# Kernel optimization log

Hardware: AMD Instinct MI355X
Metric: run time of the kernel (lower is better)

## Reference

```python
import jax, jax.numpy as jnp
import numpy as np

HEADS = 20


def _sdpa(q, k, v):
    # q: [B,H,Sq,D], k/v: [B,H,Sk,D]
    scale = 1.0 / jnp.sqrt(jnp.asarray(q.shape[-1], q.dtype))
    scores = jnp.einsum('bhqd,bhkd->bhqk', q, k) * scale
    probs = jax.nn.softmax(scores, axis=-1)
    return jnp.einsum('bhqk,bhkd->bhqd', probs, v)


def _split_heads(x, B, H):
    # [B,S,H*D] -> [B,H,S,D]
    S = x.shape[1]
    D = x.shape[2] // H
    return x.reshape(B, S, H, D).transpose(0, 2, 1, 3)


def setup_inputs() -> dict:
    key = jax.random.key(0)
    ks = jax.random.split(key, 10)
    B, S, C = 4, 4096, 1280
    T, Lid, X = 77, 32, 2048
    sc = lambda fan_in: 1.0 / np.sqrt(fan_in)
    return {
        'hidden_states': jax.random.normal(ks[0], (B, S, C), jnp.float32),
        'encoder_hidden_states': jax.random.normal(ks[1], (B, T, X), jnp.float32),
        'id_embedding': jax.random.normal(ks[2], (B, Lid, X), jnp.float32),
        'Wq': jax.random.normal(ks[3], (C, C), jnp.float32) * sc(C),
        'Wk': jax.random.normal(ks[4], (C, X), jnp.float32) * sc(X),
        'Wv': jax.random.normal(ks[5], (C, X), jnp.float32) * sc(X),
        'Wik': jax.random.normal(ks[6], (C, X), jnp.float32) * sc(X),
        'Wiv': jax.random.normal(ks[7], (C, X), jnp.float32) * sc(X),
        'Wo': jax.random.normal(ks[8], (C, C), jnp.float32) * sc(C),
        'bo': jnp.zeros((C,), jnp.float32),
    }


def reference(hidden_states, encoder_hidden_states, id_embedding,
              Wq, Wk, Wv, Wik, Wiv, Wo, bo):
    id_scale = 1.0
    B, S, C = hidden_states.shape
    H = HEADS
    residual = hidden_states

    q = _split_heads(hidden_states @ Wq.T, B, H)              # [B,H,S,D]
    k = _split_heads(encoder_hidden_states @ Wk.T, B, H)      # [B,H,T,D]
    v = _split_heads(encoder_hidden_states @ Wv.T, B, H)

    cross = _sdpa(q, k, v)                                    # [B,H,S,D]

    id_k = _split_heads(id_embedding @ Wik.T, B, H)           # [B,H,Lid,D]
    id_v = _split_heads(id_embedding @ Wiv.T, B, H)
    id_out = _sdpa(q, id_k, id_v)                             # [B,H,S,D]

    combined = cross + id_scale * id_out
    combined = combined.transpose(0, 2, 1, 3).reshape(B, S, C)

    out = combined @ Wo.T + bo
    out = out + residual  # residual_connection=True, rescale_output_factor=1.0
    return out
```

## Files before the change

kernel.cpp:

```cpp
#include <hip/hip_runtime.h>

typedef short short8 __attribute__((ext_vector_type(8)));
typedef unsigned short ushort8 __attribute__((ext_vector_type(8)));
typedef float float4v __attribute__((ext_vector_type(4)));

__device__ __forceinline__ unsigned short f2bf(float f) {
    union { float f; unsigned u; } v; v.f = f;
    unsigned r = v.u + 0x7fffu + ((v.u >> 16) & 1u);
    return (unsigned short)(r >> 16);
}

__device__ __forceinline__ void async_copy16(const void* g, void* l) {
    __builtin_amdgcn_global_load_lds(
        (__attribute__((address_space(1))) void*)g,
        (__attribute__((address_space(3))) void*)l,
        16, 0, 0);
}

__global__ __launch_bounds__(256) void cast_bf16_kernel(
        const float* __restrict__ in, unsigned short* __restrict__ out, int n) {
    int i4 = (blockIdx.x * 256 + threadIdx.x) * 4;
    if (i4 < n) {
        float4 f = *(const float4*)(in + i4);
        ushort4 u;
        u.x = f2bf(f.x); u.y = f2bf(f.y); u.z = f2bf(f.z); u.w = f2bf(f.w);
        *(ushort4*)(out + i4) = u;
    }
}

__global__ __launch_bounds__(256) void cast_enc_pad_kernel(
        const float* __restrict__ in, unsigned short* __restrict__ out) {
    int i4 = blockIdx.x * 256 + threadIdx.x;
    if (i4 < 4 * 77 * 2048 / 4) {
        const int per_b = 77 * 2048 / 4;
        int b = i4 / per_b;
        int rem = i4 - b * per_b;
        float4 f = *(const float4*)(in + (size_t)i4 * 4);
        ushort4 u;
        u.x = f2bf(f.x); u.y = f2bf(f.y); u.z = f2bf(f.z); u.w = f2bf(f.w);
        *(ushort4*)(out + ((size_t)b * (96 * 2048 / 4) + rem) * 4) = u;
    }
}

struct CastBatch {
    const float* src[8];
    unsigned short* dst[8];
    int n[8];
};
__global__ __launch_bounds__(256) void cast_batch_kernel(CastBatch cb) {
    const int t = blockIdx.y;
    const int n = cb.n[t];
    int i4 = (blockIdx.x * 256 + threadIdx.x) * 4;
    if (i4 < n) {
        float4 f = *(const float4*)(cb.src[t] + i4);
        ushort4 u;
        u.x = f2bf(f.x); u.y = f2bf(f.y); u.z = f2bf(f.z); u.w = f2bf(f.w);
        *(ushort4*)(cb.dst[t] + i4) = u;
    }
}

__global__ __launch_bounds__(256) void gemm_kv4_kernel(
        const unsigned short* __restrict__ Aenc,
        const unsigned short* __restrict__ Aid,
        const unsigned short* __restrict__ Wk,
        const unsigned short* __restrict__ Wv,
        const unsigned short* __restrict__ Wik,
        const unsigned short* __restrict__ Wiv,
        unsigned short* __restrict__ Kb, unsigned short* __restrict__ Vb,
        unsigned short* __restrict__ IKb, unsigned short* __restrict__ IVb,
        int N, int K) {
    const int z = blockIdx.z;
    const int bm = blockIdx.x * 64;
    const int Mrows = (z < 2) ? 384 : 128;
    if (bm >= Mrows) return;
    const unsigned short* A = (z < 2) ? Aenc : Aid;
    const unsigned short* B = (z == 0) ? Wk : (z == 1) ? Wv : (z == 2) ? Wik : Wiv;
    unsigned short* C = (z == 0) ? Kb : (z == 1) ? Vb : (z == 2) ? IKb : IVb;
    const int bn = blockIdx.y * 128;

    __shared__ unsigned short As[64 * 64];
    __shared__ unsigned short Bs[128 * 64];

    const int tid  = threadIdx.x;
    const int lane = tid & 63;
    const int wave = tid >> 6;
    const int wm   = (wave >> 1) * 32;
    const int wn   = (wave & 1) * 64;
    const int lr   = lane & 15;
    const int lq   = lane >> 4;

    float4v acc[2][4] = {};

    const unsigned short* aptr[2];
    const unsigned short* bptr[4];
    #pragma unroll
    for (int r = 0; r < 2; ++r) {
        const int linear = r * 256 + tid;
        const int row = linear >> 3;
        const int c = (linear & 7) ^ (row & 7);
        aptr[r] = A + (size_t)(bm + row) * K + c * 8;
    }
    #pragma unroll
    for (int r = 0; r < 4; ++r) {
        const int linear = r * 256 + tid;
        const int row = linear >> 3;
        const int c = (linear & 7) ^ (row & 7);
        bptr[r] = B + (size_t)(bn + row) * K + c * 8;
    }

    for (int ks = 0; ks < K; ks += 64) {
        #pragma unroll
        for (int r = 0; r < 2; ++r)
            async_copy16(aptr[r] + ks, (char*)As + (size_t)(r * 256 + tid) * 16);
        #pragma unroll
        for (int r = 0; r < 4; ++r)
            async_copy16(bptr[r] + ks, (char*)Bs + (size_t)(r * 256 + tid) * 16);
        __syncthreads();

        #pragma unroll
        for (int kw = 0; kw < 2; ++kw) {
            short8 af[2], bfr[4];
            #pragma unroll
            for (int i = 0; i < 2; ++i) {
                const int row = wm + i * 16 + lr;
                af[i] = *(const short8*)(As + row * 64 + (((kw << 2) | lq) ^ (row & 7)) * 8);
            }
            #pragma unroll
            for (int j = 0; j < 4; ++j) {
                const int row = wn + j * 16 + lr;
                bfr[j] = *(const short8*)(Bs + row * 64 + (((kw << 2) | lq) ^ (row & 7)) * 8);
            }
            #pragma unroll
            for (int i = 0; i < 2; ++i)
                #pragma unroll
                for (int j = 0; j < 4; ++j)
                    acc[i][j] = __builtin_amdgcn_mfma_f32_16x16x32_bf16(
                                    af[i], bfr[j], acc[i][j], 0, 0, 0);
        }
        __syncthreads();
    }

    #pragma unroll
    for (int i = 0; i < 2; ++i) {
        #pragma unroll
        for (int r = 0; r < 4; ++r) {
            const int row = bm + wm + i * 16 + lq * 4 + r;
            const size_t base = (size_t)row * N;
            #pragma unroll
            for (int j = 0; j < 4; ++j) {
                const int col = bn + wn + j * 16 + lr;
                C[base + col] = f2bf(acc[i][j][r]);
            }
        }
    }
}

template<int EPI>
__global__ __launch_bounds__(512, 2) void gemm320_kernel(
        const unsigned short* __restrict__ A,
        const unsigned short* __restrict__ B,
        float* __restrict__ Cf,
        unsigned short* __restrict__ Cb,
        const float* __restrict__ bias,
        const float* __restrict__ resid,
        int N, int K, int tn) {
    __shared__ unsigned short As[2][256 * 32];
    __shared__ unsigned short Bs[2][320 * 32];

    const int tid  = threadIdx.x;
    const int lane = tid & 63;
    const int wave = tid >> 6;
    const int wm   = (wave >> 1) * 64;
    const int wn   = (wave & 1) * 160;
    const int l15  = lane & 15;
    const int lq   = lane >> 4;

    int wg = blockIdx.x;
    const int q = gridDim.x >> 3;
    wg = (wg & 7) * q + (wg >> 3);
    const int mt = wg / tn;
    const int nt = wg - mt * tn;
    const int bm = mt * 256;
    const int bn = nt * 320;

    float4v acc[4][10] = {};

    const unsigned short* aS[2];
    const unsigned short* bS[2];
    const unsigned short* bS2;
    int dA[2], dB[2], dB2;
    #pragma unroll
    for (int g = 0; g < 2; ++g) {
        const int d = g * 512 + tid;
        const int row = d >> 2;
        const int c = (d & 3) ^ ((row >> 1) & 3);
        aS[g] = A + (size_t)(bm + row) * K + c * 8;
        bS[g] = B + (size_t)(bn + row) * K + c * 8;
        dA[g] = d * 16;
        dB[g] = d * 16;
    }
    {
        const int t2 = tid & 255;
        const int d = 1024 + t2;
        const int row = d >> 2;
        const int c = (d & 3) ^ ((row >> 1) & 3);
        bS2 = B + (size_t)(bn + row) * K + c * 8;
        dB2 = d * 16;
    }

    auto stage = [&](int t) {
        const int b = t & 1;
        #pragma unroll
        for (int g = 0; g < 2; ++g)
            async_copy16(aS[g] + t * 32, (char*)&As[b][0] + dA[g]);
        #pragma unroll
        for (int g = 0; g < 2; ++g)
            async_copy16(bS[g] + t * 32, (char*)&Bs[b][0] + dB[g]);
        if (wave < 4)
            async_copy16(bS2 + t * 32, (char*)&Bs[b][0] + dB2);
    };

    const int NT = K >> 5;
    stage(0);
    stage(1);

    for (int t = 0; t < NT; ++t) {
        const int cur = t & 1;
        if (t == NT - 1) {
            asm volatile("s_waitcnt vmcnt(0)" ::: "memory");
        } else if (wave < 4) {
            asm volatile("s_waitcnt vmcnt(5)" ::: "memory");
        } else {
            asm volatile("s_waitcnt vmcnt(4)" ::: "memory");
        }
        __builtin_amdgcn_s_barrier();
        __builtin_amdgcn_sched_barrier(0);

        short8 af[4], bf[10];
        #pragma unroll
        for (int i = 0; i < 4; ++i) {
            const int row = wm + i * 16 + l15;
            af[i] = *(const short8*)(&As[cur][row * 32 + ((lq ^ ((row >> 1) & 3)) << 3)]);
        }
        #pragma unroll
        for (int j = 0; j < 10; ++j) {
            const int row = wn + j * 16 + l15;
            bf[j] = *(const short8*)(&Bs[cur][row * 32 + ((lq ^ ((row >> 1) & 3)) << 3)]);
        }
        asm volatile("s_waitcnt lgkmcnt(0)" ::: "memory");
        __builtin_amdgcn_sched_barrier(0);
        if (t < NT - 2) {
            __builtin_amdgcn_s_barrier();
            stage(t + 2);
        }
        __builtin_amdgcn_s_setprio(1);
        #pragma unroll
        for (int i = 0; i < 4; ++i)
            #pragma unroll
            for (int j = 0; j < 10; ++j)
                acc[i][j] = __builtin_amdgcn_mfma_f32_16x16x32_bf16(
                                af[i], bf[j], acc[i][j], 0, 0, 0);
        __builtin_amdgcn_s_setprio(0);
    }

    #pragma unroll
    for (int i = 0; i < 4; ++i) {
        #pragma unroll
        for (int r = 0; r < 4; ++r) {
            const int row = bm + wm + i * 16 + lq * 4 + r;
            const size_t base = (size_t)row * N;
            #pragma unroll
            for (int j = 0; j < 10; ++j) {
                const int col = bn + wn + j * 16 + l15;
                const float v = acc[i][j][r];
                const size_t idx = base + col;
                if (EPI == 2)      Cf[idx] = v + bias[col] + resid[idx];
                else if (EPI == 1) Cb[idx] = f2bf(v);
                else               Cf[idx] = v;
            }
        }
    }
}

#define VT_STRIDE 136
__global__ __launch_bounds__(256) void attn_mfma_kernel(
        const unsigned short* __restrict__ Q,
        const unsigned short* __restrict__ Kb,
        const unsigned short* __restrict__ Vb,
        const unsigned short* __restrict__ IKb,
        const unsigned short* __restrict__ IVb,
        unsigned short* __restrict__ Cmb) {
    const int b = blockIdx.z;
    const int h = blockIdx.y;
    const int hoff = h * 64;
    const int qbase = blockIdx.x * 64;
    const int tid = threadIdx.x;
    const int lane = tid & 63;
    const int wave = tid >> 6;
    const int l15 = lane & 15;
    const int quad = lane >> 4;

    __shared__ unsigned short Vt[64 * VT_STRIDE];
    __shared__ unsigned short Pl[64 * VT_STRIDE];

    for (int i = tid; i < 96 * 8; i += 256) {
        const int c = i / 96;
        const int key = i - c * 96;
        short8 v = *(const short8*)(Vb + (size_t)(b * 96 + key) * 1280 + hoff + c * 8);
        #pragma unroll
        for (int j = 0; j < 8; ++j)
            Vt[(c * 8 + j) * VT_STRIDE + key] = (unsigned short)v[j];
    }
    {
        const int c = tid >> 5;
        const int key = tid & 31;
        short8 v = *(const short8*)(IVb + (size_t)(b * 32 + key) * 1280 + hoff + c * 8);
        #pragma unroll
        for (int j = 0; j < 8; ++j)
            Vt[(c * 8 + j) * VT_STRIDE + 96 + key] = (unsigned short)v[j];
    }
    __syncthreads();

    const int qrow = b * 4096 + qbase + wave * 16 + l15;
    const unsigned short* qp = Q + (size_t)qrow * 1280 + hoff + quad * 8;
    const short8 aQ0 = *(const short8*)(qp);
    const short8 aQ1 = *(const short8*)(qp + 32);

    const float scale = 0.125f;
    float lC[4] = {0.f, 0.f, 0.f, 0.f};
    float lI[4] = {0.f, 0.f, 0.f, 0.f};

    #pragma unroll
    for (int t = 0; t < 5; ++t) {
        const unsigned short* kp = Kb + (size_t)(b * 96 + t * 16 + l15) * 1280 + hoff + quad * 8;
        const short8 bK0 = *(const short8*)(kp);
        const short8 bK1 = *(const short8*)(kp + 32);
        float4v s = {};
        s = __builtin_amdgcn_mfma_f32_16x16x32_bf16(aQ0, bK0, s, 0, 0, 0);
        s = __builtin_amdgcn_mfma_f32_16x16x32_bf16(aQ1, bK1, s, 0, 0, 0);
        #pragma unroll
        for (int r = 0; r < 4; ++r) {
            float p = __expf(s[r] * scale);
            if (t == 4 && l15 >= 13) p = 0.f;
            lC[r] += p;
            Pl[(wave * 16 + quad * 4 + r) * VT_STRIDE + t * 16 + l15] = f2bf(p);
        }
    }
    #pragma unroll
    for (int r = 0; r < 4; ++r)
        Pl[(wave * 16 + quad * 4 + r) * VT_STRIDE + 80 + l15] = 0;

    #pragma unroll
    for (int t = 0; t < 2; ++t) {
        const unsigned short* kp = IKb + (size_t)(b * 32 + t * 16 + l15) * 1280 + hoff + quad * 8;
        const short8 bK0 = *(const short8*)(kp);
        const short8 bK1 = *(const short8*)(kp + 32);
        float4v s = {};
        s = __builtin_amdgcn_mfma_f32_16x16x32_bf16(aQ0, bK0, s, 0, 0, 0);
        s = __builtin_amdgcn_mfma_f32_16x16x32_bf16(aQ1, bK1, s, 0, 0, 0);
        #pragma unroll
        for (int r = 0; r < 4; ++r) {
            const float p = __expf(s[r] * scale);
            lI[r] += p;
            Pl[(wave * 16 + quad * 4 + r) * VT_STRIDE + 96 + t * 16 + l15] = f2bf(p);
        }
    }

    #pragma unroll
    for (int m = 1; m <= 8; m <<= 1) {
        #pragma unroll
        for (int r = 0; r < 4; ++r) {
            lC[r] += __shfl_xor(lC[r], m);
            lI[r] += __shfl_xor(lI[r], m);
        }
    }
    __syncthreads();

    float4v oC[4] = {};
    float4v oI[4] = {};
    #pragma unroll
    for (int kt = 0; kt < 3; ++kt) {
        const short8 aP = *(const short8*)(Pl + (wave * 16 + l15) * VT_STRIDE + kt * 32 + quad * 8);
        #pragma unroll
        for (int td = 0; td < 4; ++td) {
            const short8 bV = *(const short8*)(Vt + (td * 16 + l15) * VT_STRIDE + kt * 32 + quad * 8);
            oC[td] = __builtin_amdgcn_mfma_f32_16x16x32_bf16(aP, bV, oC[td], 0, 0, 0);
        }
    }
    {
        const short8 aP = *(const short8*)(Pl + (wave * 16 + l15) * VT_STRIDE + 96 + quad * 8);
        #pragma unroll
        for (int td = 0; td < 4; ++td) {
            const short8 bV = *(const short8*)(Vt + (td * 16 + l15) * VT_STRIDE + 96 + quad * 8);
            oI[td] = __builtin_amdgcn_mfma_f32_16x16x32_bf16(aP, bV, oI[td], 0, 0, 0);
        }
    }

    float rc[4], ri[4];
    #pragma unroll
    for (int r = 0; r < 4; ++r) { rc[r] = 1.f / lC[r]; ri[r] = 1.f / lI[r]; }

    #pragma unroll
    for (int td = 0; td < 4; ++td) {
        #pragma unroll
        for (int r = 0; r < 4; ++r) {
            const int row = b * 4096 + qbase + wave * 16 + quad * 4 + r;
            const int col = hoff + td * 16 + l15;
            Cmb[(size_t)row * 1280 + col] = f2bf(oC[td][r] * rc[r] + oI[td][r] * ri[r]);
        }
    }
}

extern "C" void kernel_launch(void* const* d_in, const int* in_sizes, int n_in,
                              void* d_out, int out_size, void* d_ws, size_t ws_size,
                              hipStream_t stream) {
    const float* hs  = (const float*)d_in[0];
    const float* enc = (const float*)d_in[1];
    const float* idm = (const float*)d_in[2];
    const float* Wq  = (const float*)d_in[3];
    const float* Wk  = (const float*)d_in[4];
    const float* Wv  = (const float*)d_in[5];
    const float* Wik = (const float*)d_in[6];
    const float* Wiv = (const float*)d_in[7];
    const float* Wo  = (const float*)d_in[8];
    const float* bo  = (const float*)d_in[9];
    float* out = (float*)d_out;

    char* ws = (char*)d_ws;
    size_t off = 0;
    auto carve = [&](size_t bytes) {
        char* p = ws + off;
        off += (bytes + 255) & ~(size_t)255;
        return p;
    };

    unsigned short* Xh   = (unsigned short*)carve(16384ULL * 1280 * 2);
    unsigned short* Wq_b = (unsigned short*)carve(1280ULL * 1280 * 2);
    unsigned short* Wk_b = (unsigned short*)carve(1280ULL * 2048 * 2);
    unsigned short* Wv_b = (unsigned short*)carve(1280ULL * 2048 * 2);
    unsigned short* Wik_b= (unsigned short*)carve(1280ULL * 2048 * 2);
    unsigned short* Wiv_b= (unsigned short*)carve(1280ULL * 2048 * 2);
    unsigned short* Wo_b = (unsigned short*)carve(1280ULL * 1280 * 2);
    unsigned short* Encb = (unsigned short*)carve(384ULL * 2048 * 2);
    unsigned short* Idb  = (unsigned short*)carve(128ULL * 2048 * 2);
    unsigned short* Qb   = (unsigned short*)carve(16384ULL * 1280 * 2);
    unsigned short* Kb   = (unsigned short*)carve(384ULL * 1280 * 2);
    unsigned short* Vb   = (unsigned short*)carve(384ULL * 1280 * 2);
    unsigned short* IKb  = (unsigned short*)carve(128ULL * 1280 * 2);
    unsigned short* IVb  = (unsigned short*)carve(128ULL * 1280 * 2);
    (void)ws_size; (void)in_sizes; (void)n_in; (void)out_size;

    cast_bf16_kernel<<<(4 * 4096 * 1280 / 4 + 255) / 256, 256, 0, stream>>>(
        hs, Xh, 4 * 4096 * 1280);
    cast_enc_pad_kernel<<<(4 * 77 * 2048 / 4 + 255) / 256, 256, 0, stream>>>(enc, Encb);

    CastBatch cb;
    cb.src[0] = Wq;  cb.dst[0] = Wq_b;  cb.n[0] = 1280 * 1280;
    cb.src[1] = Wk;  cb.dst[1] = Wk_b;  cb.n[1] = 1280 * 2048;
    cb.src[2] = Wv;  cb.dst[2] = Wv_b;  cb.n[2] = 1280 * 2048;
    cb.src[3] = Wik; cb.dst[3] = Wik_b; cb.n[3] = 1280 * 2048;
    cb.src[4] = Wiv; cb.dst[4] = Wiv_b; cb.n[4] = 1280 * 2048;
    cb.src[5] = Wo;  cb.dst[5] = Wo_b;  cb.n[5] = 1280 * 1280;
    cb.src[6] = idm; cb.dst[6] = Idb;   cb.n[6] = 4 * 32 * 2048;
    cb.src[7] = nullptr; cb.dst[7] = nullptr; cb.n[7] = 0;
    cast_batch_kernel<<<dim3((1280 * 2048 / 4 + 255) / 256, 7), 256, 0, stream>>>(cb);

    gemm320_kernel<1><<<dim3(64 * 4), 512, 0, stream>>>(
        Xh, Wq_b, nullptr, Qb, nullptr, nullptr, 1280, 1280, 4);

    gemm_kv4_kernel<<<dim3(6, 10, 4), 256, 0, stream>>>(
        Encb, Idb, Wk_b, Wv_b, Wik_b, Wiv_b, Kb, Vb, IKb, IVb, 1280, 2048);

    attn_mfma_kernel<<<dim3(64, 20, 4), 256, 0, stream>>>(Qb, Kb, Vb, IKb, IVb, Xh);

    gemm320_kernel<2><<<dim3(64 * 4), 512, 0, stream>>>(
        Xh, Wo_b, out, nullptr, bo, hs, 1280, 1280, 4);
}
```

Before: 423.7 us.

## Merge cast kernels into one launch and deepen GEMM LDS pipeline

Replaces the three fp32-to-bf16 cast launches with one flat kernel that maps each thread to a source and destination by index range. This removes two launch gaps and the idle blocks of the 2D batched cast. Separately, gemm320 moves from double to quadruple LDS buffering with a prefetch distance of three stages and adjusted vmcnt waits, to hide more global-load latency. The larger LDS footprint, roughly 144KB per block, may lower occupancy against the launch_bounds(512,2) target.

```diff
diff --git a/kernel.cpp b/kernel.cpp
--- a/kernel.cpp
+++ b/kernel.cpp
@@ -17,46 +17,41 @@
         16, 0, 0);
 }
 
-__global__ __launch_bounds__(256) void cast_bf16_kernel(
-        const float* __restrict__ in, unsigned short* __restrict__ out, int n) {
-    int i4 = (blockIdx.x * 256 + threadIdx.x) * 4;
-    if (i4 < n) {
-        float4 f = *(const float4*)(in + i4);
+__global__ __launch_bounds__(256) void cast_all_kernel(
+        const float* __restrict__ hs,  const float* __restrict__ enc,
+        const float* __restrict__ idm, const float* __restrict__ Wq,
+        const float* __restrict__ Wk,  const float* __restrict__ Wv,
+        const float* __restrict__ Wik, const float* __restrict__ Wiv,
+        const float* __restrict__ Wo,
+        unsigned short* __restrict__ Xh,    unsigned short* __restrict__ Encb,
+        unsigned short* __restrict__ Idb,   unsigned short* __restrict__ Wq_b,
+        unsigned short* __restrict__ Wk_b,  unsigned short* __restrict__ Wv_b,
+        unsigned short* __restrict__ Wik_b, unsigned short* __restrict__ Wiv_b,
+        unsigned short* __restrict__ Wo_b) {
+    const int g = blockIdx.x * 256 + threadIdx.x;
+    const float* src; unsigned short* dst; int l4;
+    if (g < 5242880)      { src = hs;  dst = Xh;    l4 = g; }
+    else if (g < 5652480) { src = Wq;  dst = Wq_b;  l4 = g - 5242880; }
+    else if (g < 6307840) { src = Wk;  dst = Wk_b;  l4 = g - 5652480; }
+    else if (g < 6963200) { src = Wv;  dst = Wv_b;  l4 = g - 6307840; }
+    else if (g < 7618560) { src = Wik; dst = Wik_b; l4 = g - 6963200; }
+    else if (g < 8273920) { src = Wiv; dst = Wiv_b; l4 = g - 7618560; }
+    else if (g < 8683520) { src = Wo;  dst = Wo_b;  l4 = g - 8273920; }
+    else if (g < 8749056) { src = idm; dst = Idb;   l4 = g - 8683520; }
+    else {
+        const int e = g - 8749056;
+        const int b = e / 39424;
+        const int rem = e - b * 39424;
+        float4 f = *(const float4*)(enc + (size_t)e * 4);
         ushort4 u;
         u.x = f2bf(f.x); u.y = f2bf(f.y); u.z = f2bf(f.z); u.w = f2bf(f.w);
-        *(ushort4*)(out + i4) = u;
-    }
-}
-
-__global__ __launch_bounds__(256) void cast_enc_pad_kernel(
-        const float* __restrict__ in, unsigned short* __restrict__ out) {
-    int i4 = blockIdx.x * 256 + threadIdx.x;
-    if (i4 < 4 * 77 * 2048 / 4) {
-        const int per_b = 77 * 2048 / 4;
-        int b = i4 / per_b;
-        int rem = i4 - b * per_b;
-        float4 f = *(const float4*)(in + (size_t)i4 * 4);
-        ushort4 u;
-        u.x = f2bf(f.x); u.y = f2bf(f.y); u.z = f2bf(f.z); u.w = f2bf(f.w);
-        *(ushort4*)(out + ((size_t)b * (96 * 2048 / 4) + rem) * 4) = u;
-    }
-}
-
-struct CastBatch {
-    const float* src[8];
-    unsigned short* dst[8];
-    int n[8];
-};
-__global__ __launch_bounds__(256) void cast_batch_kernel(CastBatch cb) {
-    const int t = blockIdx.y;
-    const int n = cb.n[t];
-    int i4 = (blockIdx.x * 256 + threadIdx.x) * 4;
-    if (i4 < n) {
-        float4 f = *(const float4*)(cb.src[t] + i4);
-        ushort4 u;
-        u.x = f2bf(f.x); u.y = f2bf(f.y); u.z = f2bf(f.z); u.w = f2bf(f.w);
-        *(ushort4*)(cb.dst[t] + i4) = u;
-    }
+        *(ushort4*)(Encb + ((size_t)b * 49152 + rem) * 4) = u;
+        return;
+    }
+    float4 f = *(const float4*)(src + (size_t)l4 * 4);
+    ushort4 u;
+    u.x = f2bf(f.x); u.y = f2bf(f.y); u.z = f2bf(f.z); u.w = f2bf(f.w);
+    *(ushort4*)(dst + (size_t)l4 * 4) = u;
 }
 
 __global__ __launch_bounds__(256) void gemm_kv4_kernel(
@@ -164,8 +159,8 @@
         const float* __restrict__ bias,
         const float* __restrict__ resid,
         int N, int K, int tn) {
-    __shared__ unsigned short As[2][256 * 32];
-    __shared__ unsigned short Bs[2][320 * 32];
+    __shared__ unsigned short As[4][256 * 32];
+    __shared__ unsigned short Bs[4][320 * 32];
 
     const int tid  = threadIdx.x;
     const int lane = tid & 63;
@@ -209,7 +204,7 @@
     }
 
     auto stage = [&](int t) {
-        const int b = t & 1;
+        const int b = t & 3;
         #pragma unroll
         for (int g = 0; g < 2; ++g)
             async_copy16(aS[g] + t * 32, (char*)&As[b][0] + dA[g]);
@@ -223,15 +218,18 @@
     const int NT = K >> 5;
     stage(0);
     stage(1);
+    stage(2);
 
     for (int t = 0; t < NT; ++t) {
-        const int cur = t & 1;
-        if (t == NT - 1) {
+        const int cur = t & 3;
+        if (t < NT - 2) {
+            if (wave < 4) { asm volatile("s_waitcnt vmcnt(10)" ::: "memory"); }
+            else          { asm volatile("s_waitcnt vmcnt(8)"  ::: "memory"); }
+        } else if (t == NT - 2) {
+            if (wave < 4) { asm volatile("s_waitcnt vmcnt(5)"  ::: "memory"); }
+            else          { asm volatile("s_waitcnt vmcnt(4)"  ::: "memory"); }
+        } else {
             asm volatile("s_waitcnt vmcnt(0)" ::: "memory");
-        } else if (wave < 4) {
-            asm volatile("s_waitcnt vmcnt(5)" ::: "memory");
-        } else {
-            asm volatile("s_waitcnt vmcnt(4)" ::: "memory");
         }
         __builtin_amdgcn_s_barrier();
         __builtin_amdgcn_sched_barrier(0);
@@ -249,9 +247,9 @@
         }
         asm volatile("s_waitcnt lgkmcnt(0)" ::: "memory");
         __builtin_amdgcn_sched_barrier(0);
-        if (t < NT - 2) {
+        if (t < NT - 3) {
             __builtin_amdgcn_s_barrier();
-            stage(t + 2);
+            stage(t + 3);
         }
         __builtin_amdgcn_s_setprio(1);
         #pragma unroll
@@ -450,20 +448,9 @@
     unsigned short* IVb  = (unsigned short*)carve(128ULL * 1280 * 2);
     (void)ws_size; (void)in_sizes; (void)n_in; (void)out_size;
 
-    cast_bf16_kernel<<<(4 * 4096 * 1280 / 4 + 255) / 256, 256, 0, stream>>>(
-        hs, Xh, 4 * 4096 * 1280);
-    cast_enc_pad_kernel<<<(4 * 77 * 2048 / 4 + 255) / 256, 256, 0, stream>>>(enc, Encb);
-
-    CastBatch cb;
-    cb.src[0] = Wq;  cb.dst[0] = Wq_b;  cb.n[0] = 1280 * 1280;
-    cb.src[1] = Wk;  cb.dst[1] = Wk_b;  cb.n[1] = 1280 * 2048;
-    cb.src[2] = Wv;  cb.dst[2] = Wv_b;  cb.n[2] = 1280 * 2048;
-    cb.src[3] = Wik; cb.dst[3] = Wik_b; cb.n[3] = 1280 * 2048;
-    cb.src[4] = Wiv; cb.dst[4] = Wiv_b; cb.n[4] = 1280 * 2048;
-    cb.src[5] = Wo;  cb.dst[5] = Wo_b;  cb.n[5] = 1280 * 1280;
-    cb.src[6] = idm; cb.dst[6] = Idb;   cb.n[6] = 4 * 32 * 2048;
-    cb.src[7] = nullptr; cb.dst[7] = nullptr; cb.n[7] = 0;
-    cast_batch_kernel<<<dim3((1280 * 2048 / 4 + 255) / 256, 7), 256, 0, stream>>>(cb);
+    cast_all_kernel<<<34792, 256, 0, stream>>>(
+        hs, enc, idm, Wq, Wk, Wv, Wik, Wiv, Wo,
+        Xh, Encb, Idb, Wq_b, Wk_b, Wv_b, Wik_b, Wiv_b, Wo_b);
 
     gemm320_kernel<1><<<dim3(64 * 4), 512, 0, stream>>>(
         Xh, Wq_b, nullptr, Qb, nullptr, nullptr, 1280, 1280, 4);
```

Result: no change. 416.8 us (-1.6%).
